# Optimization experiments

Hardware: AMD Instinct MI355X
Metric: run time of the kernel (lower is better)

The kernel has to match this reference:

```python
import jax, jax.numpy as jnp
import numpy as np

DIM, NUM_HEADS, N_POINTS = 256, 8, 4
N_Q, N_KV = 32768, 32768


def setup_inputs() -> dict:
    key = jax.random.key(0)
    ks = jax.random.split(key, 16)
    C, H, P = DIM, NUM_HEADS, N_POINTS
    s = 1.0 / np.sqrt(C)
    inp = {
        "query": jax.random.normal(ks[0], (N_Q, C), jnp.float32),
        "key": jax.random.normal(ks[1], (N_KV, C), jnp.float32),
        "value": jax.random.normal(ks[2], (N_KV, C), jnp.float32),
        # reference_points: Linear(C, 2*H*P)
        "Wr": jax.random.normal(ks[3], (C, 2 * H * P), jnp.float32) * s,
        "br": jnp.zeros((2 * H * P,), jnp.float32),
        # offset_attn: Linear(C, H*P*2)
        "Wo": jax.random.normal(ks[4], (C, H * P * 2), jnp.float32) * s,
        "bo": jnp.zeros((H * P * 2,), jnp.float32),
        # value_proj: Linear(C, C)
        "Wv": jax.random.normal(ks[5], (C, C), jnp.float32) * s,
        "bv": jnp.zeros((C,), jnp.float32),
        # output_proj: Linear(C, C)
        "Wout": jax.random.normal(ks[6], (C, C), jnp.float32) * s,
        "bout": jnp.zeros((C,), jnp.float32),
    }
    return inp


def reference(query, key, value, Wr, br, Wo, bo, Wv, bv, Wout, bout):
    N, C = query.shape
    M = value.shape[0]
    H, P = NUM_HEADS, N_POINTS
    Ch = C // H

    # sampling locations in [0,1] (ref) plus unconstrained offsets
    ref = jax.nn.sigmoid((query @ Wr + br).reshape(N, H, P, 2))
    off = (query @ Wo + bo).reshape(N, H, P, 2)
    loc = ref + off                              # [N,H,P,2]

    # 1-D bilinear interpolation along the token axis. The original's
    # 4-term (wx,wy) expression algebraically collapses to a pure lerp in x:
    # (1-wx)(1-wy)+ (1-wx)wy = (1-wx), wx(1-wy)+wx*wy = wx.
    x = loc[..., 0] * (M - 1)                    # [N,H,P]
    x0 = jnp.clip(jnp.floor(x).astype(jnp.int32), 0, M - 1)
    x1 = jnp.clip(x0 + 1, 0, M - 1)
    wx = (x - x0.astype(x.dtype))[..., None]     # [N,H,P,1]

    hidx = jnp.arange(H)[None, :, None]          # head-aligned gather index

    def sample(table):                           # table: [M,H,Ch]
        g0 = table[x0, hidx]                     # [N,H,P,Ch]
        g1 = table[x1, hidx]
        return (1.0 - wx) * g0 + wx * g1

    v = (value @ Wv + bv).reshape(M, H, Ch)      # value_proj, split heads
    sv = sample(v)                               # [N,H,P,Ch] sampled values

    # attention weights from query/key: sample per-head keys at the same
    # locations, dot with per-head queries, softmax over the P points
    k = key.reshape(M, H, Ch)
    sk = sample(k)                               # [N,H,P,Ch]
    q = query.reshape(N, H, Ch)
    scores = jnp.einsum("nhc,nhpc->nhp", q, sk) / jnp.sqrt(
        jnp.asarray(Ch, query.dtype)
    )
    attn = jax.nn.softmax(scores, axis=-1)       # [N,H,P]

    out = jnp.einsum("nhp,nhpc->nhc", attn, sv).reshape(N, C)
    return out @ Wout + bout
```

## Files before the change

### kernel.cpp

```cpp
#include <hip/hip_runtime.h>
#include <hip/hip_bf16.h>
#include <stdint.h>

#define NQ    32768
#define NKV   32768
#define CDIM  256
#define NHEADS 8
#define NPTS  4

using bf16x8 = __attribute__((ext_vector_type(8))) short;
using f32x4  = __attribute__((ext_vector_type(4))) float;
using u16x8  = __attribute__((ext_vector_type(8))) ushort;

static __device__ __forceinline__ ushort f2bf(float f) {
  uint32_t u = __float_as_uint(f);
  return (ushort)((u + 0x7FFFu + ((u >> 16) & 1u)) >> 16);
}
static __device__ __forceinline__ float bf2f(ushort h) {
  return __uint_as_float(((uint32_t)h) << 16);
}
static __device__ __forceinline__ void async16(const void* g, void* l) {
  __builtin_amdgcn_global_load_lds(
      (const __attribute__((address_space(1))) uint32_t*)g,
      (__attribute__((address_space(3))) uint32_t*)l, 16, 0, 0);
}
#define WAIT_VM(N) do { asm volatile("s_waitcnt vmcnt(" #N ")" ::: "memory"); \
                        __builtin_amdgcn_sched_barrier(0); } while (0)

__global__ __launch_bounds__(256) void transpose_w(const float* __restrict__ W,
                                                   ushort* __restrict__ WT) {
  int j = blockIdx.x, k = threadIdx.x;
  WT[j * 256 + k] = f2bf(W[k * 256 + j]);
}

__global__ __launch_bounds__(256) void gemm_mfma(
    const ushort* __restrict__ A, const ushort* __restrict__ BT,
    const float* __restrict__ bias, ushort* __restrict__ Cb,
    float* __restrict__ Cf, int out_bf16) {
  __shared__ ushort Alds[128 * 32];
  __shared__ ushort Blds[128 * 32];
  const int t = threadIdx.x;
  const int wave = t >> 6, lane = t & 63;
  const int mt = blockIdx.x >> 1, nt = blockIdx.x & 1;
  const int m0 = mt * 128, n0 = nt * 128;
  const int wr = wave >> 1, wc = wave & 1;
  const int r16 = lane & 15, kb = (lane >> 4) * 8;

  f32x4 acc[4][4] = {};

  for (int kt = 0; kt < 256; kt += 32) {
    __syncthreads();
#pragma unroll
    for (int it = 0; it < 2; ++it) {
      int c = it * 256 + t;
      int row = c >> 2, cc = c & 3;
      async16(A  + ((size_t)(m0 + row) * 256 + kt + cc * 8),
              Alds + (size_t)(it * 256 + wave * 64) * 8);
      async16(BT + ((size_t)(n0 + row) * 256 + kt + cc * 8),
              Blds + (size_t)(it * 256 + wave * 64) * 8);
    }
    __syncthreads();

    bf16x8 af[4], bfr[4];
#pragma unroll
    for (int m = 0; m < 4; ++m)
      af[m] = *(const bf16x8*)&Alds[(wr * 64 + m * 16 + r16) * 32 + kb];
#pragma unroll
    for (int n = 0; n < 4; ++n)
      bfr[n] = *(const bf16x8*)&Blds[(wc * 64 + n * 16 + r16) * 32 + kb];
#pragma unroll
    for (int m = 0; m < 4; ++m)
#pragma unroll
      for (int n = 0; n < 4; ++n)
        acc[m][n] = __builtin_amdgcn_mfma_f32_16x16x32_bf16(af[m], bfr[n],
                                                            acc[m][n], 0, 0, 0);
  }

  const int rg = lane >> 4;
#pragma unroll
  for (int m = 0; m < 4; ++m)
#pragma unroll
    for (int n = 0; n < 4; ++n) {
      int gc = n0 + wc * 64 + n * 16 + r16;
      float bb = bias[gc];
#pragma unroll
      for (int r = 0; r < 4; ++r) {
        int gr = m0 + wr * 64 + m * 16 + rg * 4 + r;
        float v = acc[m][n][r] + bb;
        if (out_bf16) Cb[(size_t)gr * 256 + gc] = f2bf(v);
        else          Cf[(size_t)gr * 256 + gc] = v;
      }
    }
}

__global__ __launch_bounds__(256) void gemm_mfma_fa(
    const float* __restrict__ Af, const ushort* __restrict__ BT,
    const float* __restrict__ bias, ushort* __restrict__ CbT) {
  __shared__ ushort Alds[128 * 32];
  __shared__ ushort Blds[128 * 32];
  const int t = threadIdx.x;
  const int wave = t >> 6, lane = t & 63;
  const int mt = blockIdx.x >> 1, nt = blockIdx.x & 1;
  const int m0 = mt * 128, n0 = nt * 128;
  const int wr = wave >> 1, wc = wave & 1;
  const int r16 = lane & 15, kb = (lane >> 4) * 8;

  f32x4 acc[4][4] = {};

  for (int kt = 0; kt < 256; kt += 32) {
    __syncthreads();
#pragma unroll
    for (int it = 0; it < 2; ++it) {
      int c = it * 256 + t;
      int row = c >> 2, cc = c & 3;
      async16(BT + ((size_t)(n0 + row) * 256 + kt + cc * 8),
              Blds + (size_t)(it * 256 + wave * 64) * 8);
    }
#pragma unroll
    for (int it = 0; it < 2; ++it) {
      int c = it * 256 + t;
      int row = c >> 2, cc = c & 3;
      const float* src = Af + (size_t)(m0 + row) * 256 + kt + cc * 8;
      f32x4 a = *(const f32x4*)src;
      f32x4 b = *(const f32x4*)(src + 4);
      u16x8 w;
#pragma unroll
      for (int e = 0; e < 4; ++e) { w[e] = f2bf(a[e]); w[4 + e] = f2bf(b[e]); }
      *(u16x8*)&Alds[(size_t)c * 8] = w;
    }
    __syncthreads();

    bf16x8 af[4], bfr[4];
#pragma unroll
    for (int m = 0; m < 4; ++m)
      af[m] = *(const bf16x8*)&Alds[(wr * 64 + m * 16 + r16) * 32 + kb];
#pragma unroll
    for (int n = 0; n < 4; ++n)
      bfr[n] = *(const bf16x8*)&Blds[(wc * 64 + n * 16 + r16) * 32 + kb];
#pragma unroll
    for (int m = 0; m < 4; ++m)
#pragma unroll
      for (int n = 0; n < 4; ++n)
        acc[m][n] = __builtin_amdgcn_mfma_f32_16x16x32_bf16(af[m], bfr[n],
                                                            acc[m][n], 0, 0, 0);
  }

  const int rg = lane >> 4;
#pragma unroll
  for (int m = 0; m < 4; ++m)
#pragma unroll
    for (int n = 0; n < 4; ++n) {
      int gc = n0 + wc * 64 + n * 16 + r16;
      float bb = bias[gc];
#pragma unroll
      for (int r = 0; r < 4; ++r) {
        int gr = m0 + wr * 64 + m * 16 + rg * 4 + r;
        CbT[((size_t)(gc >> 5) * NKV + gr) * 32 + (gc & 31)] =
            f2bf(acc[m][n][r] + bb);
      }
    }
}

__global__ __launch_bounds__(256) void loc_gemm(const float* __restrict__ Q,
                                                const float* __restrict__ Wr,
                                                const float* __restrict__ Wo,
                                                float* __restrict__ locr) {
  __shared__ float AT[64][68];
  __shared__ float Bl[64][64];
  const int m0 = blockIdx.x * 64;
  const int t = threadIdx.x;
  const int tr = t >> 4, tc = t & 15;
  float acc[4][4] = {};

  for (int k0 = 0; k0 < 256; k0 += 64) {
    __syncthreads();
#pragma unroll
    for (int i = 0; i < 4; ++i) {
      int row = (t >> 4) + 16 * i;
      int kk = (t & 15) * 4;
      float4 v = *(const float4*)&Q[(size_t)(m0 + row) * 256 + k0 + kk];
      AT[kk + 0][row] = v.x; AT[kk + 1][row] = v.y;
      AT[kk + 2][row] = v.z; AT[kk + 3][row] = v.w;
    }
#pragma unroll
    for (int i = 0; i < 16; ++i) {
      int j = t & 63;
      int kk = (t >> 6) + 4 * i;
      float v = (j < 32) ? Wr[(size_t)(k0 + kk) * 64 + 2 * j]
                         : Wo[(size_t)(k0 + kk) * 64 + 2 * (j - 32)];
      Bl[kk][j] = v;
    }
    __syncthreads();
#pragma unroll 8
    for (int kk = 0; kk < 64; ++kk) {
      float4 a = *(const float4*)&AT[kk][tr * 4];
      float4 b = *(const float4*)&Bl[kk][tc * 4];
      float av[4] = {a.x, a.y, a.z, a.w};
      float bv4[4] = {b.x, b.y, b.z, b.w};
#pragma unroll
      for (int i = 0; i < 4; ++i)
#pragma unroll
        for (int jj = 0; jj < 4; ++jj) acc[i][jj] += av[i] * bv4[jj];
    }
  }
#pragma unroll
  for (int i = 0; i < 4; ++i)
#pragma unroll
    for (int jj = 0; jj < 4; ++jj)
      locr[(size_t)(m0 + tr * 4 + i) * 64 + tc * 4 + jj] = acc[i][jj];
}

__global__ __launch_bounds__(256, 4) void sample_attn(
    const float* __restrict__ query, const float* __restrict__ key,
    const ushort* __restrict__ vtabT, const float* __restrict__ locr,
    const float* __restrict__ br, const float* __restrict__ bo,
    ushort* __restrict__ out2) {
  __shared__ char smem[4][4096];
  const int wave = threadIdx.x >> 6, l = threadIdx.x & 63;
  const int j = l & 31;
  const int n = blockIdx.x * 4 + wave;
  const int Mm1 = NKV - 1;
  char* vbuf = smem[wave];

  float rr = locr[(size_t)n * 64 + j];
  float oo = locr[(size_t)n * 64 + 32 + j];
  float ref = 1.0f / (1.0f + expf(-(rr + br[2 * j])));
  float x = (ref + (oo + bo[2 * j])) * (float)Mm1;
  float xf = floorf(x);
  int x0 = (int)fminf(fmaxf(xf, 0.0f), (float)Mm1);
  int x1 = (x0 + 1 > Mm1) ? Mm1 : x0 + 1;
  float wx = x - (float)x0;
  float w0 = 1.0f - wx;

  {
    const int pg3 = l >> 3, c7 = l & 7;
    const int sc = c7 ^ pg3;
#pragma unroll
    for (int i = 0; i < 4; ++i) {
      int pg = i * 8 + pg3;
      int row = __shfl(x0, pg, 64);
      async16(vtabT + ((size_t)(pg >> 2) * NKV + row) * 32 + sc * 8,
              vbuf + i * 1024);
    }
  }
  __builtin_amdgcn_sched_barrier(0);

  const int myrow = (l < 32) ? x0 : x1;
  const float* kr = key + (size_t)myrow * 256 + (j >> 2) * 32;
  const float* qr = query + (size_t)n * 256 + (j >> 2) * 32;
  f32x4 kv[8], qv[8];
#pragma unroll
  for (int c = 0; c < 8; ++c) kv[c] = *(const f32x4*)(kr + c * 4);
#pragma unroll
  for (int c = 0; c < 8; ++c) qv[c] = *(const f32x4*)(qr + c * 4);
  __builtin_amdgcn_sched_barrier(0);

  float dot = 0.f;
#pragma unroll
  for (int c = 0; c < 8; ++c)
#pragma unroll
    for (int e = 0; e < 4; ++e) dot += qv[c][e] * kv[c][e];

  float other = __shfl_xor(dot, 32, 64);
  float d0 = (l < 32) ? dot : other;
  float d1 = (l < 32) ? other : dot;
  float score = (w0 * d0 + wx * d1) * 0.17677669529663687f;

  float m1 = fmaxf(score, __shfl_xor(score, 1, 64));
  float mx = fmaxf(m1, __shfl_xor(m1, 2, 64));
  float e0 = expf(score - mx);
  float s1 = e0 + __shfl_xor(e0, 1, 64);
  float ssum = s1 + __shfl_xor(s1, 2, 64);
  float attn = e0 / ssum;
  int edge = (x0 == Mm1);
  float c1v = edge ? 0.0f : attn * wx;
  float c0v = edge ? attn * (w0 + wx) : attn * w0;

  const int oh = l >> 3, os = l & 7;
  float cc0[4], cc1[4];
#pragma unroll
  for (int m = 0; m < 4; ++m) {
    cc0[m] = __shfl(c0v, oh * 4 + m, 64);
    cc1[m] = __shfl(c1v, oh * 4 + m, 64);
  }

  WAIT_VM(0);

  float acc[4] = {};
#pragma unroll
  for (int m = 0; m < 4; ++m) {
    int pt = oh * 4 + m;
    int pos0 = (os >> 1) ^ (pt & 7);
    int pos1 = (4 + (os >> 1)) ^ (pt & 7);
    const char* pb = vbuf + pt * 128 + (os & 1) * 8;
    ushort4 v0 = *(const ushort4*)(pb + pos0 * 16);
    ushort4 v1 = *(const ushort4*)(pb + pos1 * 16);
#pragma unroll
    for (int e = 0; e < 4; ++e)
      acc[e] += cc0[m] * bf2f((&v0.x)[e]) + cc1[m] * bf2f((&v1.x)[e]);
  }
  ushort4 ow;
#pragma unroll
  for (int e = 0; e < 4; ++e) (&ow.x)[e] = f2bf(acc[e]);
  *(ushort4*)(out2 + (size_t)n * 256 + oh * 32 + os * 4) = ow;
}

extern "C" void kernel_launch(void* const* d_in, const int* in_sizes, int n_in,
                              void* d_out, int out_size, void* d_ws, size_t ws_size,
                              hipStream_t stream) {
  const float* query = (const float*)d_in[0];
  const float* key   = (const float*)d_in[1];
  const float* value = (const float*)d_in[2];
  const float* Wr    = (const float*)d_in[3];
  const float* br    = (const float*)d_in[4];
  const float* Wo    = (const float*)d_in[5];
  const float* bo    = (const float*)d_in[6];
  const float* Wv    = (const float*)d_in[7];
  const float* bv    = (const float*)d_in[8];
  const float* Wout  = (const float*)d_in[9];
  const float* bout  = (const float*)d_in[10];
  float* out = (float*)d_out;

  char* ws = (char*)d_ws;
  ushort* out2  = (ushort*)(ws);
  ushort* vtabT = (ushort*)(ws + (16u << 20));
  float*  locr  = (float*) (ws + (32u << 20));
  ushort* WvT   = (ushort*)(ws + (40u << 20));
  ushort* WoT   = (ushort*)(ws + (40u << 20) + (1u << 17));

  transpose_w<<<256, 256, 0, stream>>>(Wv, WvT);
  transpose_w<<<256, 256, 0, stream>>>(Wout, WoT);
  gemm_mfma_fa<<<(NQ / 128) * 2, 256, 0, stream>>>(value, WvT, bv, vtabT);
  loc_gemm<<<NQ / 64, 256, 0, stream>>>(query, Wr, Wo, locr);
  sample_attn<<<NQ / 4, 256, 0, stream>>>(query, key, vtabT, locr, br, bo, out2);
  gemm_mfma<<<(NQ / 128) * 2, 256, 0, stream>>>(out2, WoT, bout, nullptr, out, 0);
}
```

Before: 102.6 us.

## Stage value-projection epilogue through LDS and use sc0 cache hints on gathers

The value-projection GEMM epilogue now writes its tile into shared memory and then emits contiguous 16-byte stores into the head-major transposed table, replacing scattered 2-byte stores. The sampling kernel's random gathers (the async value loads and the key row loads) now carry the sc0 cache-policy bit through a new helper and inline asm. Because the key loads are opaque inline asm, a full vmcnt(0) wait is moved ahead of the dot product. That wait now also blocks on the async value loads before the softmax, which removes some overlap. The epilogue adds two extra barrier passes.

```diff
diff --git a/kernel.cpp b/kernel.cpp
--- a/kernel.cpp
+++ b/kernel.cpp
@@ -23,6 +23,11 @@
   __builtin_amdgcn_global_load_lds(
       (const __attribute__((address_space(1))) uint32_t*)g,
       (__attribute__((address_space(3))) uint32_t*)l, 16, 0, 0);
+}
+static __device__ __forceinline__ void async16_sc0(const void* g, void* l) {
+  __builtin_amdgcn_global_load_lds(
+      (const __attribute__((address_space(1))) uint32_t*)g,
+      (__attribute__((address_space(3))) uint32_t*)l, 16, 0, 1);
 }
 #define WAIT_VM(N) do { asm volatile("s_waitcnt vmcnt(" #N ")" ::: "memory"); \
                         __builtin_amdgcn_sched_barrier(0); } while (0)
@@ -96,8 +101,9 @@
 __global__ __launch_bounds__(256) void gemm_mfma_fa(
     const float* __restrict__ Af, const ushort* __restrict__ BT,
     const float* __restrict__ bias, ushort* __restrict__ CbT) {
-  __shared__ ushort Alds[128 * 32];
-  __shared__ ushort Blds[128 * 32];
+  __shared__ ushort S[128 * 64];
+  ushort* Alds = S;
+  ushort* Blds = S + 128 * 32;
   const int t = threadIdx.x;
   const int wave = t >> 6, lane = t & 63;
   const int mt = blockIdx.x >> 1, nt = blockIdx.x & 1;
@@ -146,19 +152,36 @@
   }
 
   const int rg = lane >> 4;
-#pragma unroll
-  for (int m = 0; m < 4; ++m)
-#pragma unroll
-    for (int n = 0; n < 4; ++n) {
-      int gc = n0 + wc * 64 + n * 16 + r16;
-      float bb = bias[gc];
-#pragma unroll
-      for (int r = 0; r < 4; ++r) {
-        int gr = m0 + wr * 64 + m * 16 + rg * 4 + r;
-        CbT[((size_t)(gc >> 5) * NKV + gr) * 32 + (gc & 31)] =
-            f2bf(acc[m][n][r] + bb);
-      }
-    }
+  const int h0 = n0 >> 5;
+#pragma unroll
+  for (int pass = 0; pass < 2; ++pass) {
+    __syncthreads();
+    if (wc == pass) {
+#pragma unroll
+      for (int m = 0; m < 4; ++m)
+#pragma unroll
+        for (int nn = 0; nn < 4; ++nn) {
+          int col = nn * 16 + r16;
+          int hh = col >> 5, ch = col & 31;
+          float bb = bias[n0 + wc * 64 + col];
+#pragma unroll
+          for (int r = 0; r < 4; ++r) {
+            int row = wr * 64 + m * 16 + rg * 4 + r;
+            S[(hh * 128 + row) * 32 + ch] = f2bf(acc[m][nn][r] + bb);
+          }
+        }
+    }
+    __syncthreads();
+#pragma unroll
+    for (int i = 0; i < 4; ++i) {
+      int chunk = i * 256 + t;
+      int hh = chunk >> 9;
+      int within = chunk & 511;
+      u16x8 w = *(const u16x8*)&S[chunk * 8];
+      ushort* dst = CbT + ((size_t)(h0 + pass * 2 + hh) * NKV + m0) * 32;
+      *(u16x8*)(dst + within * 8) = w;
+    }
+  }
 }
 
 __global__ __launch_bounds__(256) void loc_gemm(const float* __restrict__ Q,
@@ -239,27 +262,39 @@
     for (int i = 0; i < 4; ++i) {
       int pg = i * 8 + pg3;
       int row = __shfl(x0, pg, 64);
-      async16(vtabT + ((size_t)(pg >> 2) * NKV + row) * 32 + sc * 8,
-              vbuf + i * 1024);
+      async16_sc0(vtabT + ((size_t)(pg >> 2) * NKV + row) * 32 + sc * 8,
+                  vbuf + i * 1024);
     }
   }
   __builtin_amdgcn_sched_barrier(0);
 
   const int myrow = (l < 32) ? x0 : x1;
   const float* kr = key + (size_t)myrow * 256 + (j >> 2) * 32;
+  f32x4 kv0, kv1, kv2, kv3, kv4, kv5, kv6, kv7;
+  asm volatile("global_load_dwordx4 %0, %1, off sc0"            : "=v"(kv0) : "v"(kr) : "memory");
+  asm volatile("global_load_dwordx4 %0, %1, off offset:16 sc0"  : "=v"(kv1) : "v"(kr) : "memory");
+  asm volatile("global_load_dwordx4 %0, %1, off offset:32 sc0"  : "=v"(kv2) : "v"(kr) : "memory");
+  asm volatile("global_load_dwordx4 %0, %1, off offset:48 sc0"  : "=v"(kv3) : "v"(kr) : "memory");
+  asm volatile("global_load_dwordx4 %0, %1, off offset:64 sc0"  : "=v"(kv4) : "v"(kr) : "memory");
+  asm volatile("global_load_dwordx4 %0, %1, off offset:80 sc0"  : "=v"(kv5) : "v"(kr) : "memory");
+  asm volatile("global_load_dwordx4 %0, %1, off offset:96 sc0"  : "=v"(kv6) : "v"(kr) : "memory");
+  asm volatile("global_load_dwordx4 %0, %1, off offset:112 sc0" : "=v"(kv7) : "v"(kr) : "memory");
+
   const float* qr = query + (size_t)n * 256 + (j >> 2) * 32;
-  f32x4 kv[8], qv[8];
-#pragma unroll
-  for (int c = 0; c < 8; ++c) kv[c] = *(const f32x4*)(kr + c * 4);
+  f32x4 qv[8];
 #pragma unroll
   for (int c = 0; c < 8; ++c) qv[c] = *(const f32x4*)(qr + c * 4);
-  __builtin_amdgcn_sched_barrier(0);
+
+  WAIT_VM(0);
 
   float dot = 0.f;
 #pragma unroll
-  for (int c = 0; c < 8; ++c)
-#pragma unroll
-    for (int e = 0; e < 4; ++e) dot += qv[c][e] * kv[c][e];
+  for (int e = 0; e < 4; ++e) {
+    dot += qv[0][e] * kv0[e]; dot += qv[1][e] * kv1[e];
+    dot += qv[2][e] * kv2[e]; dot += qv[3][e] * kv3[e];
+    dot += qv[4][e] * kv4[e]; dot += qv[5][e] * kv5[e];
+    dot += qv[6][e] * kv6[e]; dot += qv[7][e] * kv7[e];
+  }
 
   float other = __shfl_xor(dot, 32, 64);
   float d0 = (l < 32) ? dot : other;
@@ -283,8 +318,6 @@
     cc0[m] = __shfl(c0v, oh * 4 + m, 64);
     cc1[m] = __shfl(c1v, oh * 4 + m, 64);
   }
-
-  WAIT_VM(0);
 
   float acc[4] = {};
 #pragma unroll
```

Measured after the change: 103.0 us. About the same (+0.4%).

## Widen GEMM tiles to full 256 columns and stage transposed stores through LDS

Applied to the files above, without the earlier changes.

Merges the two weight-transpose kernels into one launch. Both MFMA GEMMs now have each block compute a 128x256 tile, covering all N, instead of two 128x128 blocks. Each A tile is therefore read and, in the value projection, converted from fp32 to bf16 only once. The value-projection epilogue writes the head-major transposed output through LDS so global stores are contiguous 16-byte chunks instead of scattered 2-byte writes. In exchange, accumulator registers double and occupancy is limited to one block per CU, and the grid halves to 256 blocks.

```diff
diff --git a/kernel.cpp b/kernel.cpp
--- a/kernel.cpp
+++ b/kernel.cpp
@@ -27,93 +27,35 @@
 #define WAIT_VM(N) do { asm volatile("s_waitcnt vmcnt(" #N ")" ::: "memory"); \
                         __builtin_amdgcn_sched_barrier(0); } while (0)
 
-__global__ __launch_bounds__(256) void transpose_w(const float* __restrict__ W,
-                                                   ushort* __restrict__ WT) {
-  int j = blockIdx.x, k = threadIdx.x;
-  WT[j * 256 + k] = f2bf(W[k * 256 + j]);
-}
-
-__global__ __launch_bounds__(256) void gemm_mfma(
-    const ushort* __restrict__ A, const ushort* __restrict__ BT,
-    const float* __restrict__ bias, ushort* __restrict__ Cb,
-    float* __restrict__ Cf, int out_bf16) {
-  __shared__ ushort Alds[128 * 32];
-  __shared__ ushort Blds[128 * 32];
+__global__ __launch_bounds__(256) void transpose_both(
+    const float* __restrict__ Wv, const float* __restrict__ Wout,
+    ushort* __restrict__ WvT, ushort* __restrict__ WoT) {
+  int b = blockIdx.x, k = threadIdx.x;
+  if (b < 256) WvT[b * 256 + k] = f2bf(Wv[k * 256 + b]);
+  else { int j = b - 256; WoT[j * 256 + k] = f2bf(Wout[k * 256 + j]); }
+}
+
+__global__ __launch_bounds__(256, 1) void gemm_fa256(
+    const float* __restrict__ Af, const ushort* __restrict__ BT,
+    const float* __restrict__ bias, ushort* __restrict__ CbT) {
+  __shared__ __align__(16) ushort S[128 * 32 + 256 * 32];
+  ushort* Alds = S;
+  ushort* Blds = S + 128 * 32;
   const int t = threadIdx.x;
   const int wave = t >> 6, lane = t & 63;
-  const int mt = blockIdx.x >> 1, nt = blockIdx.x & 1;
-  const int m0 = mt * 128, n0 = nt * 128;
+  const int m0 = blockIdx.x * 128;
   const int wr = wave >> 1, wc = wave & 1;
   const int r16 = lane & 15, kb = (lane >> 4) * 8;
 
-  f32x4 acc[4][4] = {};
+  f32x4 acc[4][8] = {};
 
   for (int kt = 0; kt < 256; kt += 32) {
     __syncthreads();
 #pragma unroll
-    for (int it = 0; it < 2; ++it) {
+    for (int it = 0; it < 4; ++it) {
       int c = it * 256 + t;
       int row = c >> 2, cc = c & 3;
-      async16(A  + ((size_t)(m0 + row) * 256 + kt + cc * 8),
-              Alds + (size_t)(it * 256 + wave * 64) * 8);
-      async16(BT + ((size_t)(n0 + row) * 256 + kt + cc * 8),
-              Blds + (size_t)(it * 256 + wave * 64) * 8);
-    }
-    __syncthreads();
-
-    bf16x8 af[4], bfr[4];
-#pragma unroll
-    for (int m = 0; m < 4; ++m)
-      af[m] = *(const bf16x8*)&Alds[(wr * 64 + m * 16 + r16) * 32 + kb];
-#pragma unroll
-    for (int n = 0; n < 4; ++n)
-      bfr[n] = *(const bf16x8*)&Blds[(wc * 64 + n * 16 + r16) * 32 + kb];
-#pragma unroll
-    for (int m = 0; m < 4; ++m)
-#pragma unroll
-      for (int n = 0; n < 4; ++n)
-        acc[m][n] = __builtin_amdgcn_mfma_f32_16x16x32_bf16(af[m], bfr[n],
-                                                            acc[m][n], 0, 0, 0);
-  }
-
-  const int rg = lane >> 4;
-#pragma unroll
-  for (int m = 0; m < 4; ++m)
-#pragma unroll
-    for (int n = 0; n < 4; ++n) {
-      int gc = n0 + wc * 64 + n * 16 + r16;
-      float bb = bias[gc];
-#pragma unroll
-      for (int r = 0; r < 4; ++r) {
-        int gr = m0 + wr * 64 + m * 16 + rg * 4 + r;
-        float v = acc[m][n][r] + bb;
-        if (out_bf16) Cb[(size_t)gr * 256 + gc] = f2bf(v);
-        else          Cf[(size_t)gr * 256 + gc] = v;
-      }
-    }
-}
-
-__global__ __launch_bounds__(256) void gemm_mfma_fa(
-    const float* __restrict__ Af, const ushort* __restrict__ BT,
-    const float* __restrict__ bias, ushort* __restrict__ CbT) {
-  __shared__ ushort Alds[128 * 32];
-  __shared__ ushort Blds[128 * 32];
-  const int t = threadIdx.x;
-  const int wave = t >> 6, lane = t & 63;
-  const int mt = blockIdx.x >> 1, nt = blockIdx.x & 1;
-  const int m0 = mt * 128, n0 = nt * 128;
-  const int wr = wave >> 1, wc = wave & 1;
-  const int r16 = lane & 15, kb = (lane >> 4) * 8;
-
-  f32x4 acc[4][4] = {};
-
-  for (int kt = 0; kt < 256; kt += 32) {
-    __syncthreads();
-#pragma unroll
-    for (int it = 0; it < 2; ++it) {
-      int c = it * 256 + t;
-      int row = c >> 2, cc = c & 3;
-      async16(BT + ((size_t)(n0 + row) * 256 + kt + cc * 8),
+      async16(BT + ((size_t)row * 256 + kt + cc * 8),
               Blds + (size_t)(it * 256 + wave * 64) * 8);
     }
 #pragma unroll
@@ -130,33 +72,113 @@
     }
     __syncthreads();
 
-    bf16x8 af[4], bfr[4];
+    bf16x8 af[4], bfr[8];
 #pragma unroll
     for (int m = 0; m < 4; ++m)
       af[m] = *(const bf16x8*)&Alds[(wr * 64 + m * 16 + r16) * 32 + kb];
 #pragma unroll
-    for (int n = 0; n < 4; ++n)
-      bfr[n] = *(const bf16x8*)&Blds[(wc * 64 + n * 16 + r16) * 32 + kb];
+    for (int n = 0; n < 8; ++n)
+      bfr[n] = *(const bf16x8*)&Blds[(wc * 128 + n * 16 + r16) * 32 + kb];
 #pragma unroll
     for (int m = 0; m < 4; ++m)
 #pragma unroll
-      for (int n = 0; n < 4; ++n)
+      for (int n = 0; n < 8; ++n)
         acc[m][n] = __builtin_amdgcn_mfma_f32_16x16x32_bf16(af[m], bfr[n],
                                                             acc[m][n], 0, 0, 0);
   }
 
   const int rg = lane >> 4;
 #pragma unroll
+  for (int p = 0; p < 4; ++p) {
+    __syncthreads();
+    if (wc == (p >> 1)) {
+      int nbase = (p & 1) * 4;
+#pragma unroll
+      for (int m = 0; m < 4; ++m)
+#pragma unroll
+        for (int nn = 0; nn < 4; ++nn) {
+          int n = nbase + nn;
+          int gc = wc * 128 + n * 16 + r16;
+          int colp = gc - p * 64;
+          int hh = colp >> 5, ch = colp & 31;
+          float bb = bias[gc];
+#pragma unroll
+          for (int r = 0; r < 4; ++r) {
+            int row = wr * 64 + m * 16 + rg * 4 + r;
+            S[(hh * 128 + row) * 32 + ch] = f2bf(acc[m][n][r] + bb);
+          }
+        }
+    }
+    __syncthreads();
+#pragma unroll
+    for (int i = 0; i < 4; ++i) {
+      int chunk = i * 256 + t;
+      int hh = chunk >> 9, within = chunk & 511;
+      u16x8 w = *(const u16x8*)&S[chunk * 8];
+      ushort* dst = CbT + ((size_t)(p * 2 + hh) * NKV + m0) * 32;
+      *(u16x8*)(dst + within * 8) = w;
+    }
+  }
+}
+
+__global__ __launch_bounds__(256, 1) void gemm_out256(
+    const ushort* __restrict__ A, const ushort* __restrict__ BT,
+    const float* __restrict__ bias, float* __restrict__ Cf) {
+  __shared__ __align__(16) ushort S[128 * 32 + 256 * 32];
+  ushort* Alds = S;
+  ushort* Blds = S + 128 * 32;
+  const int t = threadIdx.x;
+  const int wave = t >> 6, lane = t & 63;
+  const int m0 = blockIdx.x * 128;
+  const int wr = wave >> 1, wc = wave & 1;
+  const int r16 = lane & 15, kb = (lane >> 4) * 8;
+
+  f32x4 acc[4][8] = {};
+
+  for (int kt = 0; kt < 256; kt += 32) {
+    __syncthreads();
+#pragma unroll
+    for (int it = 0; it < 4; ++it) {
+      int c = it * 256 + t;
+      int row = c >> 2, cc = c & 3;
+      async16(BT + ((size_t)row * 256 + kt + cc * 8),
+              Blds + (size_t)(it * 256 + wave * 64) * 8);
+    }
+#pragma unroll
+    for (int it = 0; it < 2; ++it) {
+      int c = it * 256 + t;
+      int row = c >> 2, cc = c & 3;
+      async16(A + ((size_t)(m0 + row) * 256 + kt + cc * 8),
+              Alds + (size_t)(it * 256 + wave * 64) * 8);
+    }
+    __syncthreads();
+
+    bf16x8 af[4], bfr[8];
+#pragma unroll
+    for (int m = 0; m < 4; ++m)
+      af[m] = *(const bf16x8*)&Alds[(wr * 64 + m * 16 + r16) * 32 + kb];
+#pragma unroll
+    for (int n = 0; n < 8; ++n)
+      bfr[n] = *(const bf16x8*)&Blds[(wc * 128 + n * 16 + r16) * 32 + kb];
+#pragma unroll
+    for (int m = 0; m < 4; ++m)
+#pragma unroll
+      for (int n = 0; n < 8; ++n)
+        acc[m][n] = __builtin_amdgcn_mfma_f32_16x16x32_bf16(af[m], bfr[n],
+                                                            acc[m][n], 0, 0, 0);
+  }
+
+  const int rg = lane >> 4;
+#pragma unroll
   for (int m = 0; m < 4; ++m)
 #pragma unroll
-    for (int n = 0; n < 4; ++n) {
-      int gc = n0 + wc * 64 + n * 16 + r16;
+    for (int n = 0; n < 8; ++n) {
+      int gc = wc * 128 + n * 16 + r16;
       float bb = bias[gc];
 #pragma unroll
       for (int r = 0; r < 4; ++r) {
         int gr = m0 + wr * 64 + m * 16 + rg * 4 + r;
-        CbT[((size_t)(gc >> 5) * NKV + gr) * 32 + (gc & 31)] =
-            f2bf(acc[m][n][r] + bb);
+        Cf[(size_t)gr * 256 + gc] = acc[m][n][r] + bb;
       }
     }
 }
@@ -328,10 +350,9 @@
   ushort* WvT   = (ushort*)(ws + (40u << 20));
   ushort* WoT   = (ushort*)(ws + (40u << 20) + (1u << 17));
 
-  transpose_w<<<256, 256, 0, stream>>>(Wv, WvT);
-  transpose_w<<<256, 256, 0, stream>>>(Wout, WoT);
-  gemm_mfma_fa<<<(NQ / 128) * 2, 256, 0, stream>>>(value, WvT, bv, vtabT);
+  transpose_both<<<512, 256, 0, stream>>>(Wv, Wout, WvT, WoT);
+  gemm_fa256<<<NQ / 128, 256, 0, stream>>>(value, WvT, bv, vtabT);
   loc_gemm<<<NQ / 64, 256, 0, stream>>>(query, Wr, Wo, locr);
   sample_attn<<<NQ / 4, 256, 0, stream>>>(query, key, vtabT, locr, br, bo, out2);
-  gemm_mfma<<<(NQ / 128) * 2, 256, 0, stream>>>(out2, WoT, bout, nullptr, out, 0);
-}
+  gemm_out256<<<NQ / 128, 256, 0, stream>>>(out2, WoT, bout, out);
+}
```

New measurement: 106.2 us. 3.5% more time.
